# Kernel optimization log

Measured on AMD Instinct MI355X. Metric: run time of the kernel, lower is better.

The kernel has to match this reference:

```python
import jax, jax.numpy as jnp
import numpy as np

N = 50000     # nodes
E = 800000    # edges (before self-loops)
DIN = 128     # input feature dim
DH = 16       # per-head hidden dim (layer 1)
H = 8         # heads (layer 1)
DOUT = 64     # output classes (layer 2, heads=1)


def setup_inputs() -> dict:
    key = jax.random.key(0)
    ks = jax.random.split(key, 10)
    def rn(k, shape, scale=0.1):
        return jax.random.normal(k, shape, dtype=jnp.float32) * scale
    x = jax.random.normal(ks[0], (N, DIN), dtype=jnp.float32)
    edge_index = jax.random.randint(ks[1], (2, E), 0, N, dtype=jnp.int64)
    return {
        "x": x,
        "edge_index": edge_index,
        "W1": rn(ks[2], (DIN, H * DH)),
        "a_src1": rn(ks[3], (H, DH)),
        "a_dst1": rn(ks[4], (H, DH)),
        "b1": jnp.zeros((H * DH,), jnp.float32),
        "W2": rn(ks[5], (H * DH, DOUT)),
        "a_src2": rn(ks[6], (1, DOUT)),
        "a_dst2": rn(ks[7], (1, DOUT)),
        "b2": jnp.zeros((DOUT,), jnp.float32),
    }


def gat_conv(x, src, dst, W, a_src, a_dst, b, heads, out_dim):
    """PyG-style GATConv: edge attention + segment softmax over dst + scatter-add."""
    n = x.shape[0]
    h = (x @ W).reshape(n, heads, out_dim)                 # [N, H, D]
    alpha_src = jnp.sum(h * a_src, axis=-1)                # [N, H]
    alpha_dst = jnp.sum(h * a_dst, axis=-1)                # [N, H]
    e = jax.nn.leaky_relu(alpha_src[src] + alpha_dst[dst], 0.2)  # [Etot, H]
    # numerically-stable segment softmax grouped by destination node
    m = jax.ops.segment_max(e, dst, num_segments=n)        # [N, H]
    ex = jnp.exp(e - m[dst])
    s = jax.ops.segment_sum(ex, dst, num_segments=n)       # [N, H]
    alpha = ex / (s[dst] + 1e-16)                          # [Etot, H]
    msg = h[src] * alpha[..., None]                        # [Etot, H, D]
    out = jax.ops.segment_sum(msg, dst, num_segments=n)    # [N, H, D]
    return out.reshape(n, heads * out_dim) + b


def reference(x, W1, a_src1, a_dst1, b1, W2, a_src2, a_dst2, b2, edge_index):
    # eval mode: F.dropout(p=0.6, training=False) is identity
    loop = jnp.arange(N, dtype=edge_index.dtype)
    src = jnp.concatenate([edge_index[0], loop])  # add_self_loops=True (PyG default)
    dst = jnp.concatenate([edge_index[1], loop])
    h = gat_conv(x, src, dst, W1, a_src1, a_dst1, b1, H, DH)
    h = jax.nn.elu(h)
    h = gat_conv(h, src, dst, W2, a_src2, a_dst2, b2, 1, DOUT)
    return (h, jax.nn.log_softmax(h, axis=1))
```

## Files before the change

kernel.cpp:

```cpp
#include <hip/hip_runtime.h>

#define NN 50000
#define EE 800000
#define ET (EE + NN)
#define NCH ((NN + 255) / 256)
#define DEGB ((ET + 255) / 256)
#define WPB ((128 * 128 + 128 * 64 + 255) / 256)
#define GEMB ((NN + 63) / 64)

typedef unsigned short ushort_t;
using bf16x8 = __attribute__((ext_vector_type(8))) short;
using f32x4  = __attribute__((ext_vector_type(4))) float;

__device__ __forceinline__ float bf2f(ushort_t u) {
    return __uint_as_float(((unsigned int)u) << 16);
}
__device__ __forceinline__ ushort_t f2bf(float f) {
    unsigned int u = __float_as_uint(f);
    u += 0x7fffu + ((u >> 16) & 1u);
    return (ushort_t)(u >> 16);
}
__device__ __forceinline__ float lrelu(float e) {
    return fmaxf(e, 0.f) + 0.2f * fminf(e, 0.f);
}
__device__ __forceinline__ float ldf(const void* p, int i, bool f32) {
    return f32 ? ((const float*)p)[i] : bf2f(((const ushort_t*)p)[i]);
}

__device__ __forceinline__ bool sniff_f32(const unsigned int* __restrict__ xw) {
    int lane = threadIdx.x & 63;
    float v = __uint_as_float(xw[lane]);
    float a = fabsf(v);
    bool ok = (a > 1e-6f && a < 1e6f) || v == 0.f;
    unsigned long long m = __ballot(ok);
    return __popcll(m) >= 48;
}
__device__ __forceinline__ bool sniff_i64(const int* __restrict__ eiw) {
    int lane = threadIdx.x & 63;
    unsigned long long m = __ballot(eiw[2 * lane + 1] != 0);
    return __popcll(m) <= 4;
}

__device__ __forceinline__ void edge_sd(const int* ei, int i, bool i64, int& s, int& d) {
    if (i < EE) {
        if (i64) { s = ei[2 * i]; d = ei[2 * (EE + i)]; }
        else     { s = ei[i];     d = ei[EE + i]; }
    } else {
        s = d = i - EE;
    }
}
__device__ __forceinline__ int edge_d(const int* ei, int i, bool i64) {
    if (i < EE) return i64 ? ei[2 * (EE + i)] : ei[EE + i];
    return i - EE;
}

__global__ __launch_bounds__(256) void prep_kernel(const int* __restrict__ ei, int* __restrict__ deg8,
                                                   int* __restrict__ rank,
                                                   const unsigned int* __restrict__ xw,
                                                   const void* W1v, const void* W2v,
                                                   ushort_t* __restrict__ Wt1, ushort_t* __restrict__ Wt2) {
    int b = blockIdx.x;
    if (b < DEGB) {
        bool i64 = sniff_i64(ei);
        int i = b * 256 + threadIdx.x;
        if (i >= ET) return;
        int g = b & 7;
        int d = edge_d(ei, i, i64);
        rank[i] = atomicAdd(&deg8[(size_t)g * NN + d], 1);
    } else {
        bool f32 = sniff_f32(xw);
        int i = (b - DEGB) * 256 + threadIdx.x;
        if (i < 128 * 128) {
            int k = i >> 7, nc = i & 127;
            ushort_t v = f32 ? f2bf(((const float*)W1v)[i]) : ((const ushort_t*)W1v)[i];
            Wt1[nc * 128 + k] = v;
        }
        int j = i - 128 * 128;
        if (j >= 0 && j < 128 * 64) {
            int k = j >> 6, nc = j & 63;
            ushort_t v = f32 ? f2bf(((const float*)W2v)[j]) : ((const ushort_t*)W2v)[j];
            Wt2[nc * 128 + k] = v;
        }
    }
}

#define FLG_A (1ull << 62)

__global__ __launch_bounds__(256) void scan_kernel(int* __restrict__ deg8, int* __restrict__ rowptr,
                                                   unsigned long long* __restrict__ state) {
    __shared__ int wsum[4];
    __shared__ int bpref;
    int b = blockIdx.x;
    int t = threadIdx.x;
    int node = b * 256 + t;
    int lane = t & 63, wid = t >> 6;
    int dv[8];
    int v = 0;
    if (node < NN) {
        #pragma unroll
        for (int g = 0; g < 8; ++g) {
            dv[g] = deg8[(size_t)g * NN + node];
            v += dv[g];
        }
    }
    int x = v;
    #pragma unroll
    for (int off = 1; off < 64; off <<= 1) {
        int y = __shfl_up(x, off);
        if (lane >= off) x += y;
    }
    if (lane == 63) wsum[wid] = x;
    __syncthreads();
    if (t < 4) {
        int s = wsum[t];
        #pragma unroll
        for (int off = 1; off < 4; off <<= 1) {
            int y = __shfl_up(s, off);
            if (t >= off) s += y;
        }
        wsum[t] = s;
    }
    __syncthreads();
    int total = wsum[3];
    if (t == 0) atomicExch(&state[b], FLG_A | (unsigned long long)(unsigned)total);
    if (t < 64) {
        int p = 0;
        #pragma unroll
        for (int w = 0; w < (NCH + 63) / 64; ++w) {
            int j = w * 64 + t;
            unsigned long long sv = 0;
            if (j < b) {
                do { sv = atomicAdd(&state[j], 0ull); __builtin_amdgcn_s_sleep(1); } while (!(sv >> 62));
            }
            p += (int)(unsigned)(sv & 0xffffffffull);
        }
        #pragma unroll
        for (int off = 1; off < 64; off <<= 1) p += __shfl_xor(p, off);
        if (t == 0) bpref = p;
    }
    __syncthreads();
    int excl = x - v + ((wid > 0) ? wsum[wid - 1] : 0);
    if (node < NN) {
        int run = bpref + excl;
        rowptr[node] = run;
        #pragma unroll
        for (int g = 0; g < 8; ++g) {
            deg8[(size_t)g * NN + node] = run;
            run += dv[g];
        }
    }
    if (b == NCH - 1 && t == 0) rowptr[NN] = bpref + total;
}

template <bool AEXT, int NCOL, int NH>
__device__ __forceinline__ void mgemm_body(int bid, const void* Av, const ushort_t* __restrict__ Wt,
                                           const void* a_src, const void* a_dst,
                                           ushort_t* __restrict__ outb, float* __restrict__ asrc,
                                           float* __restrict__ adst, int n, bool f32) {
    constexpr int K = 128;
    constexpr int NCT = NCOL / 16;
    bool af32 = AEXT && f32;
    int t = threadIdx.x;
    int lane = t & 63, wid = t >> 6;
    int m = lane & 15, quad = lane >> 4;
    int rbase = bid * 64 + wid * 16;
    int row = rbase + m;
    bool rok = row < n;

    bf16x8 af[4];
    if (rok) {
        if (!af32) {
            const ushort_t* ap = (const ushort_t*)Av + (size_t)row * K + quad * 8;
            #pragma unroll
            for (int kk = 0; kk < 4; ++kk) af[kk] = *(const bf16x8*)(ap + kk * 32);
        } else {
            const float* ap = (const float*)Av + (size_t)row * K + quad * 8;
            #pragma unroll
            for (int kk = 0; kk < 4; ++kk) {
                float4 q0 = *(const float4*)(ap + kk * 32);
                float4 q1 = *(const float4*)(ap + kk * 32 + 4);
                bf16x8 v;
                v[0] = (short)f2bf(q0.x); v[1] = (short)f2bf(q0.y);
                v[2] = (short)f2bf(q0.z); v[3] = (short)f2bf(q0.w);
                v[4] = (short)f2bf(q1.x); v[5] = (short)f2bf(q1.y);
                v[6] = (short)f2bf(q1.z); v[7] = (short)f2bf(q1.w);
                af[kk] = v;
            }
        }
    } else {
        #pragma unroll
        for (int kk = 0; kk < 4; ++kk) af[kk] = (bf16x8){0, 0, 0, 0, 0, 0, 0, 0};
    }

    f32x4 acc[NCT];
    #pragma unroll
    for (int c = 0; c < NCT; ++c) acc[c] = (f32x4){0.f, 0.f, 0.f, 0.f};

    const ushort_t* wp = Wt + (size_t)m * K + quad * 8;
    #pragma unroll
    for (int c = 0; c < NCT; ++c) {
        const ushort_t* wc = wp + (size_t)c * 16 * K;
        #pragma unroll
        for (int kk = 0; kk < 4; ++kk) {
            bf16x8 bf = *(const bf16x8*)(wc + kk * 32);
            acc[c] = __builtin_amdgcn_mfma_f32_16x16x32_bf16(af[kk], bf, acc[c], 0, 0, 0);
        }
    }

    int orow0 = rbase + quad * 4;
    #pragma unroll
    for (int c = 0; c < NCT; ++c) {
        #pragma unroll
        for (int r = 0; r < 4; ++r) {
            int orow = orow0 + r;
            if (orow < n) outb[(size_t)orow * NCOL + c * 16 + m] = f2bf(acc[c][r]);
        }
    }

    if (NH == 8) {
        #pragma unroll
        for (int c = 0; c < NCT; ++c) {
            float as = ldf(a_src, c * 16 + m, f32);
            float ad = ldf(a_dst, c * 16 + m, f32);
            float ps[4], pd[4];
            #pragma unroll
            for (int r = 0; r < 4; ++r) { ps[r] = acc[c][r] * as; pd[r] = acc[c][r] * ad; }
            #pragma unroll
            for (int stp = 1; stp < 16; stp <<= 1) {
                #pragma unroll
                for (int r = 0; r < 4; ++r) {
                    ps[r] += __shfl_xor(ps[r], stp);
                    pd[r] += __shfl_xor(pd[r], stp);
                }
            }
            if (m == 0) {
                #pragma unroll
                for (int r = 0; r < 4; ++r) {
                    int orow = orow0 + r;
                    if (orow < n) {
                        asrc[(size_t)orow * 8 + c] = ps[r];
                        adst[(size_t)orow * 8 + c] = pd[r];
                    }
                }
            }
        }
    } else {
        float ps[4] = {0.f, 0.f, 0.f, 0.f}, pd[4] = {0.f, 0.f, 0.f, 0.f};
        #pragma unroll
        for (int c = 0; c < NCT; ++c) {
            float as = ldf(a_src, c * 16 + m, f32);
            float ad = ldf(a_dst, c * 16 + m, f32);
            #pragma unroll
            for (int r = 0; r < 4; ++r) {
                ps[r] = fmaf(acc[c][r], as, ps[r]);
                pd[r] = fmaf(acc[c][r], ad, pd[r]);
            }
        }
        #pragma unroll
        for (int stp = 1; stp < 16; stp <<= 1) {
            #pragma unroll
            for (int r = 0; r < 4; ++r) {
                ps[r] += __shfl_xor(ps[r], stp);
                pd[r] += __shfl_xor(pd[r], stp);
            }
        }
        if (m == 0) {
            #pragma unroll
            for (int r = 0; r < 4; ++r) {
                int orow = orow0 + r;
                if (orow < n) { asrc[orow] = ps[r]; adst[orow] = pd[r]; }
            }
        }
    }
}

__global__ __launch_bounds__(256) void gemm1_fill_kernel(const void* xv, const ushort_t* __restrict__ Wt1,
                                                         const void* as1, const void* ad1,
                                                         ushort_t* __restrict__ h1b,
                                                         float* __restrict__ asrc1, float* __restrict__ adst1,
                                                         const int* __restrict__ ei,
                                                         const int* __restrict__ deg8off,
                                                         const int* __restrict__ rank, int* __restrict__ col) {
    if (blockIdx.x < GEMB) {
        bool f32 = sniff_f32((const unsigned int*)xv);
        mgemm_body<true, 128, 8>(blockIdx.x, xv, Wt1, as1, ad1, h1b, asrc1, adst1, NN, f32);
        return;
    }
    int bb = blockIdx.x - GEMB;
    bool i64 = sniff_i64(ei);
    int i = bb * 256 + threadIdx.x;
    if (i >= ET) return;
    int g = bb & 7;
    int s, d;
    edge_sd(ei, i, i64, s, d);
    col[deg8off[(size_t)g * NN + d] + rank[i]] = s;
}

__global__ __launch_bounds__(256) void mgemm2_kernel(const void* Av, const ushort_t* __restrict__ Wt,
                                                     const void* a_src, const void* a_dst,
                                                     ushort_t* __restrict__ outb, float* __restrict__ asrc,
                                                     float* __restrict__ adst, const unsigned int* __restrict__ xw) {
    bool f32 = sniff_f32(xw);
    mgemm_body<false, 64, 1>(blockIdx.x, Av, Wt, a_src, a_dst, outb, asrc, adst, NN, f32);
}

__global__ __launch_bounds__(256) void agg1_kernel(const unsigned int* __restrict__ xw,
                                                   const int* __restrict__ rowptr, const int* __restrict__ col,
                                                   const ushort_t* __restrict__ h1b,
                                                   const float* __restrict__ asrc, const float* __restrict__ adst,
                                                   const void* b1, ushort_t* __restrict__ hmidb) {
    __shared__ float wle[4][8 * 72];
    __shared__ int loff[4][64];
    bool f32 = sniff_f32(xw);
    int lane = threadIdx.x & 63, wid = threadIdx.x >> 6;
    int d = blockIdx.x * 4 + wid;
    if (d >= NN) return;
    int start = rowptr[d], end = rowptr[d + 1];
    int sub = lane & 15;
    int eg  = lane >> 4;
    int hB  = sub >> 1;
    const float4* dp = (const float4*)(adst + (size_t)d * 8);
    float4 ad0 = dp[0], ad1 = dp[1];
    const char* hb = (const char*)h1b + sub * 16;
    float acc[8] = {0.f, 0.f, 0.f, 0.f, 0.f, 0.f, 0.f, 0.f};
    float ssum = 0.f;
    for (int chunk = start; chunk < end; chunk += 64) {
        int cnt = min(64, end - chunk);
        int c = (chunk + lane < end) ? col[chunk + lane] : 0;
        loff[wid][lane] = c << 8;
        if (lane < cnt) {
            const float4* ap = (const float4*)(asrc + (size_t)c * 8);
            float4 s0 = ap[0], s1 = ap[1];
            wle[wid][0 * 72 + lane] = __expf(lrelu(s0.x + ad0.x));
            wle[wid][1 * 72 + lane] = __expf(lrelu(s0.y + ad0.y));
            wle[wid][2 * 72 + lane] = __expf(lrelu(s0.z + ad0.z));
            wle[wid][3 * 72 + lane] = __expf(lrelu(s0.w + ad0.w));
            wle[wid][4 * 72 + lane] = __expf(lrelu(s1.x + ad1.x));
            wle[wid][5 * 72 + lane] = __expf(lrelu(s1.y + ad1.y));
            wle[wid][6 * 72 + lane] = __expf(lrelu(s1.z + ad1.z));
            wle[wid][7 * 72 + lane] = __expf(lrelu(s1.w + ad1.w));
        } else {
            #pragma unroll
            for (int h = 0; h < 8; ++h) wle[wid][h * 72 + lane] = 0.f;
        }
        int niter = (cnt + 3) >> 2;
        #pragma unroll 4
        for (int jj = 0; jj < niter; ++jj) {
            int j = jj * 4 + eg;
            int off = loff[wid][j];
            float ex = wle[wid][hB * 72 + j];
            uint4 hv = *(const uint4*)(hb + off);
            ssum += ex;
            acc[0] = fmaf(ex, __uint_as_float(hv.x << 16), acc[0]);
            acc[1] = fmaf(ex, __uint_as_float(hv.x & 0xffff0000u), acc[1]);
            acc[2] = fmaf(ex, __uint_as_float(hv.y << 16), acc[2]);
            acc[3] = fmaf(ex, __uint_as_float(hv.y & 0xffff0000u), acc[3]);
            acc[4] = fmaf(ex, __uint_as_float(hv.z << 16), acc[4]);
            acc[5] = fmaf(ex, __uint_as_float(hv.z & 0xffff0000u), acc[5]);
            acc[6] = fmaf(ex, __uint_as_float(hv.w << 16), acc[6]);
            acc[7] = fmaf(ex, __uint_as_float(hv.w & 0xffff0000u), acc[7]);
        }
    }
    #pragma unroll
    for (int off = 16; off < 64; off <<= 1) {
        ssum += __shfl_xor(ssum, off);
        #pragma unroll
        for (int k = 0; k < 8; ++k) acc[k] += __shfl_xor(acc[k], off);
    }
    if (eg == 0) {
        float inv = 1.f / (ssum + 1e-16f);
        uint4 pk;
        unsigned int pw[4];
        #pragma unroll
        for (int k = 0; k < 4; ++k) {
            float o0 = fmaf(acc[2 * k],     inv, ldf(b1, sub * 8 + 2 * k,     f32));
            float o1 = fmaf(acc[2 * k + 1], inv, ldf(b1, sub * 8 + 2 * k + 1, f32));
            o0 = (o0 > 0.f) ? o0 : (__expf(o0) - 1.f);
            o1 = (o1 > 0.f) ? o1 : (__expf(o1) - 1.f);
            pw[k] = ((unsigned int)f2bf(o1) << 16) | (unsigned int)f2bf(o0);
        }
        pk.x = pw[0]; pk.y = pw[1]; pk.z = pw[2]; pk.w = pw[3];
        *(uint4*)(hmidb + (size_t)d * 128 + sub * 8) = pk;
    }
}

__global__ __launch_bounds__(256) void agg2_kernel(const unsigned int* __restrict__ xw,
                                                   const int* __restrict__ rowptr, const int* __restrict__ col,
                                                   const ushort_t* __restrict__ h2b,
                                                   const float* __restrict__ asrc, const float* __restrict__ adst,
                                                   const void* b2, float* __restrict__ out) {
    __shared__ float wle[4][64];
    __shared__ int loff[4][64];
    bool f32 = sniff_f32(xw);
    int lane = threadIdx.x & 63, wid = threadIdx.x >> 6;
    int d = blockIdx.x * 4 + wid;
    if (d >= NN) return;
    int start = rowptr[d], end = rowptr[d + 1];
    int sub = lane & 7;
    int eg  = lane >> 3;
    float ad = adst[d];
    const char* hb = (const char*)h2b + sub * 16;
    float acc[8] = {0.f, 0.f, 0.f, 0.f, 0.f, 0.f, 0.f, 0.f};
    float ssum = 0.f;
    for (int chunk = start; chunk < end; chunk += 64) {
        int cnt = min(64, end - chunk);
        int c = (chunk + lane < end) ? col[chunk + lane] : 0;
        loff[wid][lane] = c << 7;
        float e = 0.f;
        if (lane < cnt) e = __expf(lrelu(asrc[c] + ad));
        wle[wid][lane] = e;
        int niter = (cnt + 7) >> 3;
        #pragma unroll 2
        for (int jj = 0; jj < niter; ++jj) {
            int j = jj * 8 + eg;
            int off = loff[wid][j];
            float ex = wle[wid][j];
            uint4 hv = *(const uint4*)(hb + off);
            ssum += ex;
            acc[0] = fmaf(ex, __uint_as_float(hv.x << 16), acc[0]);
            acc[1] = fmaf(ex, __uint_as_float(hv.x & 0xffff0000u), acc[1]);
            acc[2] = fmaf(ex, __uint_as_float(hv.y << 16), acc[2]);
            acc[3] = fmaf(ex, __uint_as_float(hv.y & 0xffff0000u), acc[3]);
            acc[4] = fmaf(ex, __uint_as_float(hv.z << 16), acc[4]);
            acc[5] = fmaf(ex, __uint_as_float(hv.z & 0xffff0000u), acc[5]);
            acc[6] = fmaf(ex, __uint_as_float(hv.w << 16), acc[6]);
            acc[7] = fmaf(ex, __uint_as_float(hv.w & 0xffff0000u), acc[7]);
        }
    }
    #pragma unroll
    for (int off = 8; off < 64; off <<= 1) {
        ssum += __shfl_xor(ssum, off);
        #pragma unroll
        for (int k = 0; k < 8; ++k) acc[k] += __shfl_xor(acc[k], off);
    }
    if (eg == 0) {
        float inv = 1.f / (ssum + 1e-16f);
        float o[8];
        #pragma unroll
        for (int k = 0; k < 8; ++k) o[k] = fmaf(acc[k], inv, ldf(b2, sub * 8 + k, f32));
        float mm = o[0];
        #pragma unroll
        for (int k = 1; k < 8; ++k) mm = fmaxf(mm, o[k]);
        #pragma unroll
        for (int off = 1; off < 8; off <<= 1) mm = fmaxf(mm, __shfl_xor(mm, off));
        float ts = 0.f;
        #pragma unroll
        for (int k = 0; k < 8; ++k) ts += __expf(o[k] - mm);
        #pragma unroll
        for (int off = 1; off < 8; off <<= 1) ts += __shfl_xor(ts, off);
        float lg = mm + __logf(ts);
        float4 w0, w1, l0, l1;
        w0.x = o[0]; w0.y = o[1]; w0.z = o[2]; w0.w = o[3];
        w1.x = o[4]; w1.y = o[5]; w1.z = o[6]; w1.w = o[7];
        l0.x = o[0] - lg; l0.y = o[1] - lg; l0.z = o[2] - lg; l0.w = o[3] - lg;
        l1.x = o[4] - lg; l1.y = o[5] - lg; l1.z = o[6] - lg; l1.w = o[7] - lg;
        float* op = out + (size_t)d * 64 + sub * 8;
        *(float4*)op = w0;
        *(float4*)(op + 4) = w1;
        float* lp = out + (size_t)NN * 64 + (size_t)d * 64 + sub * 8;
        *(float4*)lp = l0;
        *(float4*)(lp + 4) = l1;
    }
}

extern "C" void kernel_launch(void* const* d_in, const int* in_sizes, int n_in,
                              void* d_out, int out_size, void* d_ws, size_t ws_size,
                              hipStream_t stream) {
    const void* x   = d_in[0];
    const int*  ei  = (const int*)d_in[1];
    const void* W1  = d_in[2];
    const void* as1 = d_in[3];
    const void* ad1 = d_in[4];
    const void* b1  = d_in[5];
    const void* W2  = d_in[6];
    const void* as2 = d_in[7];
    const void* ad2 = d_in[8];
    const void* b2  = d_in[9];
    float* out = (float*)d_out;

    char* w = (char*)d_ws;
    auto alloc = [&](size_t bytes) {
        void* p = (void*)w;
        w += (bytes + 255) & ~(size_t)255;
        return p;
    };
    int* deg8     = (int*)alloc((size_t)8 * NN * 4 + 4096);
    unsigned long long* state = (unsigned long long*)((char*)deg8 + (size_t)8 * NN * 4);
    int* rowptr   = (int*)alloc((size_t)(NN + 1) * 4);
    int* rank     = (int*)alloc((size_t)ET * 4);
    int* colx     = (int*)alloc((size_t)ET * 4);
    ushort_t* Wt1 = (ushort_t*)alloc((size_t)128 * 128 * 2);
    ushort_t* Wt2 = (ushort_t*)alloc((size_t)64 * 128 * 2);
    ushort_t* h1b = (ushort_t*)alloc((size_t)NN * 128 * 2);
    float* asrc1  = (float*)alloc((size_t)NN * 8 * 4);
    float* adst1  = (float*)alloc((size_t)NN * 8 * 4);
    ushort_t* hmidb = (ushort_t*)alloc((size_t)NN * 128 * 2);
    ushort_t* h2b = (ushort_t*)alloc((size_t)NN * 64 * 2);
    float* asrc2  = (float*)alloc((size_t)NN * 4);
    float* adst2  = (float*)alloc((size_t)NN * 4);

    hipMemsetAsync(deg8, 0, (size_t)8 * NN * 4 + (size_t)NCH * 8, stream);

    prep_kernel<<<DEGB + WPB, 256, 0, stream>>>(ei, deg8, rank, (const unsigned int*)x, W1, W2, Wt1, Wt2);
    scan_kernel<<<NCH, 256, 0, stream>>>(deg8, rowptr, state);
    gemm1_fill_kernel<<<GEMB + DEGB, 256, 0, stream>>>(x, Wt1, as1, ad1, h1b, asrc1, adst1,
                                                       ei, deg8, rank, colx);
    agg1_kernel<<<(NN + 3) / 4, 256, 0, stream>>>((const unsigned int*)x, rowptr, colx, h1b,
                                                  asrc1, adst1, b1, hmidb);
    mgemm2_kernel<<<GEMB, 256, 0, stream>>>((const void*)hmidb, Wt2, as2, ad2, h2b, asrc2, adst2,
                                            (const unsigned int*)x);
    agg2_kernel<<<(NN + 3) / 4, 256, 0, stream>>>((const unsigned int*)x, rowptr, colx, h2b,
                                                  asrc2, adst2, b2, out);
}
```

Before: 252.0 us.

## Split layer-1 aggregation into per-edge alpha pass and head-planar gather

Layer-1 aggregation is split into two kernels. The first computes normalized attention coefficients per edge and head and stores them as bf16 planes. The second runs one block per (node group, head) and gathers from a head-planar copy of h1 that the GEMM now writes, so each head's gather footprint is 32 bytes per node. The aim is to improve cache locality for the random gather by working through one head's features at a time. In exchange it adds an extra launch, a 13.6 MB alpha buffer written and read back, eight reloads of col per node, and a redundant exp recomputation for long rows.

New measurement: 404.8 us. +60.6%, slower.

```diff
diff --git a/kernel.cpp b/kernel.cpp
--- a/kernel.cpp
+++ b/kernel.cpp
@@ -7,6 +7,7 @@
 #define DEGB ((ET + 255) / 256)
 #define WPB ((128 * 128 + 128 * 64 + 255) / 256)
 #define GEMB ((NN + 63) / 64)
+#define NODB ((NN + 3) / 4)
 
 typedef unsigned short ushort_t;
 using bf16x8 = __attribute__((ext_vector_type(8))) short;
@@ -152,7 +153,7 @@
     if (b == NCH - 1 && t == 0) rowptr[NN] = bpref + total;
 }
 
-template <bool AEXT, int NCOL, int NH>
+template <bool AEXT, int NCOL, int NH, bool PLANE>
 __device__ __forceinline__ void mgemm_body(int bid, const void* Av, const ushort_t* __restrict__ Wt,
                                            const void* a_src, const void* a_dst,
                                            ushort_t* __restrict__ outb, float* __restrict__ asrc,
@@ -213,7 +214,10 @@
         #pragma unroll
         for (int r = 0; r < 4; ++r) {
             int orow = orow0 + r;
-            if (orow < n) outb[(size_t)orow * NCOL + c * 16 + m] = f2bf(acc[c][r]);
+            if (orow < n) {
+                if (PLANE) outb[((size_t)c * n + orow) * 16 + m] = f2bf(acc[c][r]);
+                else       outb[(size_t)orow * NCOL + c * 16 + m] = f2bf(acc[c][r]);
+            }
         }
     }
 
@@ -276,14 +280,14 @@
 
 __global__ __launch_bounds__(256) void gemm1_fill_kernel(const void* xv, const ushort_t* __restrict__ Wt1,
                                                          const void* as1, const void* ad1,
-                                                         ushort_t* __restrict__ h1b,
+                                                         ushort_t* __restrict__ h1p,
                                                          float* __restrict__ asrc1, float* __restrict__ adst1,
                                                          const int* __restrict__ ei,
                                                          const int* __restrict__ deg8off,
                                                          const int* __restrict__ rank, int* __restrict__ col) {
     if (blockIdx.x < GEMB) {
         bool f32 = sniff_f32((const unsigned int*)xv);
-        mgemm_body<true, 128, 8>(blockIdx.x, xv, Wt1, as1, ad1, h1b, asrc1, adst1, NN, f32);
+        mgemm_body<true, 128, 8, true>(blockIdx.x, xv, Wt1, as1, ad1, h1p, asrc1, adst1, NN, f32);
         return;
     }
     int bb = blockIdx.x - GEMB;
@@ -301,86 +305,143 @@
                                                      ushort_t* __restrict__ outb, float* __restrict__ asrc,
                                                      float* __restrict__ adst, const unsigned int* __restrict__ xw) {
     bool f32 = sniff_f32(xw);
-    mgemm_body<false, 64, 1>(blockIdx.x, Av, Wt, a_src, a_dst, outb, asrc, adst, NN, f32);
-}
-
-__global__ __launch_bounds__(256) void agg1_kernel(const unsigned int* __restrict__ xw,
-                                                   const int* __restrict__ rowptr, const int* __restrict__ col,
-                                                   const ushort_t* __restrict__ h1b,
-                                                   const float* __restrict__ asrc, const float* __restrict__ adst,
-                                                   const void* b1, ushort_t* __restrict__ hmidb) {
-    __shared__ float wle[4][8 * 72];
-    __shared__ int loff[4][64];
-    bool f32 = sniff_f32(xw);
+    mgemm_body<false, 64, 1, false>(blockIdx.x, Av, Wt, a_src, a_dst, outb, asrc, adst, NN, f32);
+}
+
+__global__ __launch_bounds__(256) void alpha1_kernel(const int* __restrict__ rowptr, const int* __restrict__ col,
+                                                     const float* __restrict__ asrc, const float* __restrict__ adst,
+                                                     ushort_t* __restrict__ aplane) {
     int lane = threadIdx.x & 63, wid = threadIdx.x >> 6;
     int d = blockIdx.x * 4 + wid;
     if (d >= NN) return;
     int start = rowptr[d], end = rowptr[d + 1];
-    int sub = lane & 15;
-    int eg  = lane >> 4;
-    int hB  = sub >> 1;
     const float4* dp = (const float4*)(adst + (size_t)d * 8);
     float4 ad0 = dp[0], ad1 = dp[1];
-    const char* hb = (const char*)h1b + sub * 16;
-    float acc[8] = {0.f, 0.f, 0.f, 0.f, 0.f, 0.f, 0.f, 0.f};
-    float ssum = 0.f;
+    float ss[8] = {0.f, 0.f, 0.f, 0.f, 0.f, 0.f, 0.f, 0.f};
+    float ex0[8];
     for (int chunk = start; chunk < end; chunk += 64) {
-        int cnt = min(64, end - chunk);
-        int c = (chunk + lane < end) ? col[chunk + lane] : 0;
-        loff[wid][lane] = c << 8;
-        if (lane < cnt) {
+        int idx = chunk + lane;
+        float e[8];
+        if (idx < end) {
+            int c = col[idx];
             const float4* ap = (const float4*)(asrc + (size_t)c * 8);
             float4 s0 = ap[0], s1 = ap[1];
-            wle[wid][0 * 72 + lane] = __expf(lrelu(s0.x + ad0.x));
-            wle[wid][1 * 72 + lane] = __expf(lrelu(s0.y + ad0.y));
-            wle[wid][2 * 72 + lane] = __expf(lrelu(s0.z + ad0.z));
-            wle[wid][3 * 72 + lane] = __expf(lrelu(s0.w + ad0.w));
-            wle[wid][4 * 72 + lane] = __expf(lrelu(s1.x + ad1.x));
-            wle[wid][5 * 72 + lane] = __expf(lrelu(s1.y + ad1.y));
-            wle[wid][6 * 72 + lane] = __expf(lrelu(s1.z + ad1.z));
-            wle[wid][7 * 72 + lane] = __expf(lrelu(s1.w + ad1.w));
+            e[0] = __expf(lrelu(s0.x + ad0.x));
+            e[1] = __expf(lrelu(s0.y + ad0.y));
+            e[2] = __expf(lrelu(s0.z + ad0.z));
+            e[3] = __expf(lrelu(s0.w + ad0.w));
+            e[4] = __expf(lrelu(s1.x + ad1.x));
+            e[5] = __expf(lrelu(s1.y + ad1.y));
+            e[6] = __expf(lrelu(s1.z + ad1.z));
+            e[7] = __expf(lrelu(s1.w + ad1.w));
         } else {
             #pragma unroll
-            for (int h = 0; h < 8; ++h) wle[wid][h * 72 + lane] = 0.f;
-        }
-        int niter = (cnt + 3) >> 2;
+            for (int k = 0; k < 8; ++k) e[k] = 0.f;
+        }
+        #pragma unroll
+        for (int k = 0; k < 8; ++k) ss[k] += e[k];
+        if (chunk == start) {
+            #pragma unroll
+            for (int k = 0; k < 8; ++k) ex0[k] = e[k];
+        }
+    }
+    #pragma unroll
+    for (int off = 1; off < 64; off <<= 1) {
+        #pragma unroll
+        for (int k = 0; k < 8; ++k) ss[k] += __shfl_xor(ss[k], off);
+    }
+    float inv[8];
+    #pragma unroll
+    for (int k = 0; k < 8; ++k) inv[k] = 1.f / (ss[k] + 1e-16f);
+    {
+        int idx = start + lane;
+        if (idx < end) {
+            #pragma unroll
+            for (int k = 0; k < 8; ++k)
+                aplane[(size_t)k * ET + idx] = f2bf(ex0[k] * inv[k]);
+        }
+    }
+    for (int chunk = start + 64; chunk < end; chunk += 64) {
+        int idx = chunk + lane;
+        if (idx < end) {
+            int c = col[idx];
+            const float4* ap = (const float4*)(asrc + (size_t)c * 8);
+            float4 s0 = ap[0], s1 = ap[1];
+            float e[8];
+            e[0] = __expf(lrelu(s0.x + ad0.x));
+            e[1] = __expf(lrelu(s0.y + ad0.y));
+            e[2] = __expf(lrelu(s0.z + ad0.z));
+            e[3] = __expf(lrelu(s0.w + ad0.w));
+            e[4] = __expf(lrelu(s1.x + ad1.x));
+            e[5] = __expf(lrelu(s1.y + ad1.y));
+            e[6] = __expf(lrelu(s1.z + ad1.z));
+            e[7] = __expf(lrelu(s1.w + ad1.w));
+            #pragma unroll
+            for (int k = 0; k < 8; ++k)
+                aplane[(size_t)k * ET + idx] = f2bf(e[k] * inv[k]);
+        }
+    }
+}
+
+__global__ __launch_bounds__(256) void agg1b_kernel(const unsigned int* __restrict__ xw,
+                                                    const int* __restrict__ rowptr, const int* __restrict__ col,
+                                                    const ushort_t* __restrict__ h1p,
+                                                    const ushort_t* __restrict__ aplane,
+                                                    const void* b1, ushort_t* __restrict__ hmidb) {
+    __shared__ float wal[4][64];
+    __shared__ int loff[4][64];
+    bool f32 = sniff_f32(xw);
+    int lane = threadIdx.x & 63, wid = threadIdx.x >> 6;
+    int h = blockIdx.x & 7;
+    int d = (blockIdx.x >> 3) * 4 + wid;
+    if (d >= NN) return;
+    int start = rowptr[d], end = rowptr[d + 1];
+    int el = lane >> 2, dl = lane & 3;
+    const char* pb = (const char*)(h1p + (size_t)h * NN * 16) + dl * 8;
+    const ushort_t* ap = aplane + (size_t)h * ET;
+    float a0 = 0.f, a1 = 0.f, a2 = 0.f, a3 = 0.f;
+    for (int chunk = start; chunk < end; chunk += 64) {
+        int idx = chunk + lane;
+        int cnt = min(64, end - chunk);
+        int c = (idx < end) ? __builtin_nontemporal_load(&col[idx]) : 0;
+        loff[wid][lane] = c << 5;
+        float av = 0.f;
+        if (lane < cnt) av = bf2f(__builtin_nontemporal_load(&ap[idx]));
+        wal[wid][lane] = av;
+        int niter = (cnt + 15) >> 4;
         #pragma unroll 4
         for (int jj = 0; jj < niter; ++jj) {
-            int j = jj * 4 + eg;
+            int j = jj * 16 + el;
             int off = loff[wid][j];
-            float ex = wle[wid][hB * 72 + j];
-            uint4 hv = *(const uint4*)(hb + off);
-            ssum += ex;
-            acc[0] = fmaf(ex, __uint_as_float(hv.x << 16), acc[0]);
-            acc[1] = fmaf(ex, __uint_as_float(hv.x & 0xffff0000u), acc[1]);
-            acc[2] = fmaf(ex, __uint_as_float(hv.y << 16), acc[2]);
-            acc[3] = fmaf(ex, __uint_as_float(hv.y & 0xffff0000u), acc[3]);
-            acc[4] = fmaf(ex, __uint_as_float(hv.z << 16), acc[4]);
-            acc[5] = fmaf(ex, __uint_as_float(hv.z & 0xffff0000u), acc[5]);
-            acc[6] = fmaf(ex, __uint_as_float(hv.w << 16), acc[6]);
-            acc[7] = fmaf(ex, __uint_as_float(hv.w & 0xffff0000u), acc[7]);
-        }
-    }
-    #pragma unroll
-    for (int off = 16; off < 64; off <<= 1) {
-        ssum += __shfl_xor(ssum, off);
-        #pragma unroll
-        for (int k = 0; k < 8; ++k) acc[k] += __shfl_xor(acc[k], off);
-    }
-    if (eg == 0) {
-        float inv = 1.f / (ssum + 1e-16f);
-        uint4 pk;
-        unsigned int pw[4];
-        #pragma unroll
-        for (int k = 0; k < 4; ++k) {
-            float o0 = fmaf(acc[2 * k],     inv, ldf(b1, sub * 8 + 2 * k,     f32));
-            float o1 = fmaf(acc[2 * k + 1], inv, ldf(b1, sub * 8 + 2 * k + 1, f32));
-            o0 = (o0 > 0.f) ? o0 : (__expf(o0) - 1.f);
-            o1 = (o1 > 0.f) ? o1 : (__expf(o1) - 1.f);
-            pw[k] = ((unsigned int)f2bf(o1) << 16) | (unsigned int)f2bf(o0);
-        }
-        pk.x = pw[0]; pk.y = pw[1]; pk.z = pw[2]; pk.w = pw[3];
-        *(uint4*)(hmidb + (size_t)d * 128 + sub * 8) = pk;
+            float a = wal[wid][j];
+            uint2 hv = *(const uint2*)(pb + off);
+            a0 = fmaf(a, __uint_as_float(hv.x << 16), a0);
+            a1 = fmaf(a, __uint_as_float(hv.x & 0xffff0000u), a1);
+            a2 = fmaf(a, __uint_as_float(hv.y << 16), a2);
+            a3 = fmaf(a, __uint_as_float(hv.y & 0xffff0000u), a3);
+        }
+    }
+    #pragma unroll
+    for (int off = 4; off < 64; off <<= 1) {
+        a0 += __shfl_xor(a0, off);
+        a1 += __shfl_xor(a1, off);
+        a2 += __shfl_xor(a2, off);
+        a3 += __shfl_xor(a3, off);
+    }
+    if (el == 0) {
+        int db = h * 16 + dl * 4;
+        float o0 = a0 + ldf(b1, db + 0, f32);
+        float o1 = a1 + ldf(b1, db + 1, f32);
+        float o2 = a2 + ldf(b1, db + 2, f32);
+        float o3 = a3 + ldf(b1, db + 3, f32);
+        o0 = (o0 > 0.f) ? o0 : (__expf(o0) - 1.f);
+        o1 = (o1 > 0.f) ? o1 : (__expf(o1) - 1.f);
+        o2 = (o2 > 0.f) ? o2 : (__expf(o2) - 1.f);
+        o3 = (o3 > 0.f) ? o3 : (__expf(o3) - 1.f);
+        uint2 pk;
+        pk.x = ((unsigned int)f2bf(o1) << 16) | (unsigned int)f2bf(o0);
+        pk.y = ((unsigned int)f2bf(o3) << 16) | (unsigned int)f2bf(o2);
+        *(uint2*)(hmidb + (size_t)d * 128 + db) = pk;
     }
 }
 
@@ -491,9 +552,10 @@
     int* colx     = (int*)alloc((size_t)ET * 4);
     ushort_t* Wt1 = (ushort_t*)alloc((size_t)128 * 128 * 2);
     ushort_t* Wt2 = (ushort_t*)alloc((size_t)64 * 128 * 2);
-    ushort_t* h1b = (ushort_t*)alloc((size_t)NN * 128 * 2);
+    ushort_t* h1p = (ushort_t*)alloc((size_t)8 * NN * 16 * 2);
     float* asrc1  = (float*)alloc((size_t)NN * 8 * 4);
     float* adst1  = (float*)alloc((size_t)NN * 8 * 4);
+    ushort_t* aplane = (ushort_t*)alloc((size_t)8 * ET * 2);
     ushort_t* hmidb = (ushort_t*)alloc((size_t)NN * 128 * 2);
     ushort_t* h2b = (ushort_t*)alloc((size_t)NN * 64 * 2);
     float* asrc2  = (float*)alloc((size_t)NN * 4);
@@ -503,12 +565,13 @@
 
     prep_kernel<<<DEGB + WPB, 256, 0, stream>>>(ei, deg8, rank, (const unsigned int*)x, W1, W2, Wt1, Wt2);
     scan_kernel<<<NCH, 256, 0, stream>>>(deg8, rowptr, state);
-    gemm1_fill_kernel<<<GEMB + DEGB, 256, 0, stream>>>(x, Wt1, as1, ad1, h1b, asrc1, adst1,
+    gemm1_fill_kernel<<<GEMB + DEGB, 256, 0, stream>>>(x, Wt1, as1, ad1, h1p, asrc1, adst1,
                                                        ei, deg8, rank, colx);
-    agg1_kernel<<<(NN + 3) / 4, 256, 0, stream>>>((const unsigned int*)x, rowptr, colx, h1b,
-                                                  asrc1, adst1, b1, hmidb);
+    alpha1_kernel<<<NODB, 256, 0, stream>>>(rowptr, colx, asrc1, adst1, aplane);
+    agg1b_kernel<<<NODB * 8, 256, 0, stream>>>((const unsigned int*)x, rowptr, colx, h1p,
+                                               aplane, b1, hmidb);
     mgemm2_kernel<<<GEMB, 256, 0, stream>>>((const void*)hmidb, Wt2, as2, ad2, h2b, asrc2, adst2,
                                             (const unsigned int*)x);
-    agg2_kernel<<<(NN + 3) / 4, 256, 0, stream>>>((const unsigned int*)x, rowptr, colx, h2b,
-                                                  asrc2, adst2, b2, out);
-}
+    agg2_kernel<<<NODB, 256, 0, stream>>>((const unsigned int*)x, rowptr, colx, h2b,
+                                          asrc2, adst2, b2, out);
+}
```

## Fuse layer-2 GEMM into agg1 epilogue and vectorize edge preprocessing by 4

Applied to the files above, without the earlier changes.

The layer-2 projection and its attention logits are now computed inside agg1 with per-wave FMA dot products from shared memory. This removes the hmidb intermediate buffer, the mgemm2 launch and the round trip of the intermediate through memory. agg1's gather is restructured so each lane handles 2 features per edge, iterating serially over all edges instead of 4 edge groups with 8 features each. The degree-count and CSR-fill kernels now process 4 edges per thread with vector loads. The trade-offs are that the second GEMM runs on scalar FMAs instead of MFMA, and the agg1 inner loop has less edge-level parallelism.

Measured after the change: 373.9 us. +48.3%, slower.

```diff
diff --git a/kernel.cpp b/kernel.cpp
--- a/kernel.cpp
+++ b/kernel.cpp
@@ -4,9 +4,10 @@
 #define EE 800000
 #define ET (EE + NN)
 #define NCH ((NN + 255) / 256)
-#define DEGB ((ET + 255) / 256)
+#define DEG4B ((ET + 1023) / 1024)
 #define WPB ((128 * 128 + 128 * 64 + 255) / 256)
 #define GEMB ((NN + 63) / 64)
+#define NODB ((NN + 3) / 4)
 
 typedef unsigned short ushort_t;
 using bf16x8 = __attribute__((ext_vector_type(8))) short;
@@ -41,17 +42,35 @@
     return __popcll(m) <= 4;
 }
 
-__device__ __forceinline__ void edge_sd(const int* ei, int i, bool i64, int& s, int& d) {
-    if (i < EE) {
-        if (i64) { s = ei[2 * i]; d = ei[2 * (EE + i)]; }
-        else     { s = ei[i];     d = ei[EE + i]; }
+__device__ __forceinline__ void edge_d4(const int* __restrict__ ei, int i0, bool i64, int (&d)[4]) {
+    if (i0 < EE) {
+        if (i64) {
+            int4 r = *(const int4*)(ei + 2 * (size_t)(EE + i0));
+            int4 u = *(const int4*)(ei + 2 * (size_t)(EE + i0) + 4);
+            d[0] = r.x; d[1] = r.z; d[2] = u.x; d[3] = u.z;
+        } else {
+            int4 dv = *(const int4*)(ei + (size_t)EE + i0);
+            d[0] = dv.x; d[1] = dv.y; d[2] = dv.z; d[3] = dv.w;
+        }
     } else {
-        s = d = i - EE;
-    }
-}
-__device__ __forceinline__ int edge_d(const int* ei, int i, bool i64) {
-    if (i < EE) return i64 ? ei[2 * (EE + i)] : ei[EE + i];
-    return i - EE;
+        #pragma unroll
+        for (int e = 0; e < 4; ++e) d[e] = i0 + e - EE;
+    }
+}
+__device__ __forceinline__ void edge_s4(const int* __restrict__ ei, int i0, bool i64, int (&s)[4]) {
+    if (i0 < EE) {
+        if (i64) {
+            int4 p = *(const int4*)(ei + 2 * (size_t)i0);
+            int4 q = *(const int4*)(ei + 2 * (size_t)i0 + 4);
+            s[0] = p.x; s[1] = p.z; s[2] = q.x; s[3] = q.z;
+        } else {
+            int4 sv = *(const int4*)(ei + (size_t)i0);
+            s[0] = sv.x; s[1] = sv.y; s[2] = sv.z; s[3] = sv.w;
+        }
+    } else {
+        #pragma unroll
+        for (int e = 0; e < 4; ++e) s[e] = i0 + e - EE;
+    }
 }
 
 __global__ __launch_bounds__(256) void prep_kernel(const int* __restrict__ ei, int* __restrict__ deg8,
@@ -60,16 +79,26 @@
                                                    const void* W1v, const void* W2v,
                                                    ushort_t* __restrict__ Wt1, ushort_t* __restrict__ Wt2) {
     int b = blockIdx.x;
-    if (b < DEGB) {
+    if (b < DEG4B) {
         bool i64 = sniff_i64(ei);
-        int i = b * 256 + threadIdx.x;
-        if (i >= ET) return;
+        int i0 = (b * 256 + threadIdx.x) * 4;
+        if (i0 >= ET) return;
         int g = b & 7;
-        int d = edge_d(ei, i, i64);
-        rank[i] = atomicAdd(&deg8[(size_t)g * NN + d], 1);
+        int d[4], r[4];
+        edge_d4(ei, i0, i64, d);
+        #pragma unroll
+        for (int e = 0; e < 4; ++e)
+            if (i0 + e < ET) r[e] = atomicAdd(&deg8[(size_t)g * NN + d[e]], 1);
+        if (i0 + 3 < ET) {
+            int4 rv; rv.x = r[0]; rv.y = r[1]; rv.z = r[2]; rv.w = r[3];
+            *(int4*)(rank + i0) = rv;
+        } else {
+            #pragma unroll
+            for (int e = 0; e < 4; ++e) if (i0 + e < ET) rank[i0 + e] = r[e];
+        }
     } else {
         bool f32 = sniff_f32(xw);
-        int i = (b - DEGB) * 256 + threadIdx.x;
+        int i = (b - DEG4B) * 256 + threadIdx.x;
         if (i < 128 * 128) {
             int k = i >> 7, nc = i & 127;
             ushort_t v = f32 ? f2bf(((const float*)W1v)[i]) : ((const ushort_t*)W1v)[i];
@@ -152,24 +181,22 @@
     if (b == NCH - 1 && t == 0) rowptr[NN] = bpref + total;
 }
 
-template <bool AEXT, int NCOL, int NH>
-__device__ __forceinline__ void mgemm_body(int bid, const void* Av, const ushort_t* __restrict__ Wt,
-                                           const void* a_src, const void* a_dst,
-                                           ushort_t* __restrict__ outb, float* __restrict__ asrc,
-                                           float* __restrict__ adst, int n, bool f32) {
+__device__ __forceinline__ void mgemm1_body(int bid, const void* Av, const ushort_t* __restrict__ Wt,
+                                            const void* a_src, const void* a_dst,
+                                            ushort_t* __restrict__ outb, float* __restrict__ asrc,
+                                            float* __restrict__ adst, bool f32) {
     constexpr int K = 128;
-    constexpr int NCT = NCOL / 16;
-    bool af32 = AEXT && f32;
+    constexpr int NCT = 8;
     int t = threadIdx.x;
     int lane = t & 63, wid = t >> 6;
     int m = lane & 15, quad = lane >> 4;
     int rbase = bid * 64 + wid * 16;
     int row = rbase + m;
-    bool rok = row < n;
+    bool rok = row < NN;
 
     bf16x8 af[4];
     if (rok) {
-        if (!af32) {
+        if (!f32) {
             const ushort_t* ap = (const ushort_t*)Av + (size_t)row * K + quad * 8;
             #pragma unroll
             for (int kk = 0; kk < 4; ++kk) af[kk] = *(const bf16x8*)(ap + kk * 32);
@@ -213,49 +240,17 @@
         #pragma unroll
         for (int r = 0; r < 4; ++r) {
             int orow = orow0 + r;
-            if (orow < n) outb[(size_t)orow * NCOL + c * 16 + m] = f2bf(acc[c][r]);
-        }
-    }
-
-    if (NH == 8) {
-        #pragma unroll
-        for (int c = 0; c < NCT; ++c) {
-            float as = ldf(a_src, c * 16 + m, f32);
-            float ad = ldf(a_dst, c * 16 + m, f32);
-            float ps[4], pd[4];
-            #pragma unroll
-            for (int r = 0; r < 4; ++r) { ps[r] = acc[c][r] * as; pd[r] = acc[c][r] * ad; }
-            #pragma unroll
-            for (int stp = 1; stp < 16; stp <<= 1) {
-                #pragma unroll
-                for (int r = 0; r < 4; ++r) {
-                    ps[r] += __shfl_xor(ps[r], stp);
-                    pd[r] += __shfl_xor(pd[r], stp);
-                }
-            }
-            if (m == 0) {
-                #pragma unroll
-                for (int r = 0; r < 4; ++r) {
-                    int orow = orow0 + r;
-                    if (orow < n) {
-                        asrc[(size_t)orow * 8 + c] = ps[r];
-                        adst[(size_t)orow * 8 + c] = pd[r];
-                    }
-                }
-            }
-        }
-    } else {
-        float ps[4] = {0.f, 0.f, 0.f, 0.f}, pd[4] = {0.f, 0.f, 0.f, 0.f};
-        #pragma unroll
-        for (int c = 0; c < NCT; ++c) {
-            float as = ldf(a_src, c * 16 + m, f32);
-            float ad = ldf(a_dst, c * 16 + m, f32);
-            #pragma unroll
-            for (int r = 0; r < 4; ++r) {
-                ps[r] = fmaf(acc[c][r], as, ps[r]);
-                pd[r] = fmaf(acc[c][r], ad, pd[r]);
-            }
-        }
+            if (orow < NN) outb[(size_t)orow * 128 + c * 16 + m] = f2bf(acc[c][r]);
+        }
+    }
+
+    #pragma unroll
+    for (int c = 0; c < NCT; ++c) {
+        float as = ldf(a_src, c * 16 + m, f32);
+        float ad = ldf(a_dst, c * 16 + m, f32);
+        float ps[4], pd[4];
+        #pragma unroll
+        for (int r = 0; r < 4; ++r) { ps[r] = acc[c][r] * as; pd[r] = acc[c][r] * ad; }
         #pragma unroll
         for (int stp = 1; stp < 16; stp <<= 1) {
             #pragma unroll
@@ -268,7 +263,10 @@
             #pragma unroll
             for (int r = 0; r < 4; ++r) {
                 int orow = orow0 + r;
-                if (orow < n) { asrc[orow] = ps[r]; adst[orow] = pd[r]; }
+                if (orow < NN) {
+                    asrc[(size_t)orow * 8 + c] = ps[r];
+                    adst[(size_t)orow * 8 + c] = pd[r];
+                }
             }
         }
     }
@@ -283,47 +281,51 @@
                                                          const int* __restrict__ rank, int* __restrict__ col) {
     if (blockIdx.x < GEMB) {
         bool f32 = sniff_f32((const unsigned int*)xv);
-        mgemm_body<true, 128, 8>(blockIdx.x, xv, Wt1, as1, ad1, h1b, asrc1, adst1, NN, f32);
+        mgemm1_body(blockIdx.x, xv, Wt1, as1, ad1, h1b, asrc1, adst1, f32);
         return;
     }
     int bb = blockIdx.x - GEMB;
     bool i64 = sniff_i64(ei);
-    int i = bb * 256 + threadIdx.x;
-    if (i >= ET) return;
+    int i0 = (bb * 256 + threadIdx.x) * 4;
+    if (i0 >= ET) return;
     int g = bb & 7;
-    int s, d;
-    edge_sd(ei, i, i64, s, d);
-    col[deg8off[(size_t)g * NN + d] + rank[i]] = s;
-}
-
-__global__ __launch_bounds__(256) void mgemm2_kernel(const void* Av, const ushort_t* __restrict__ Wt,
-                                                     const void* a_src, const void* a_dst,
-                                                     ushort_t* __restrict__ outb, float* __restrict__ asrc,
-                                                     float* __restrict__ adst, const unsigned int* __restrict__ xw) {
-    bool f32 = sniff_f32(xw);
-    mgemm_body<false, 64, 1>(blockIdx.x, Av, Wt, a_src, a_dst, outb, asrc, adst, NN, f32);
+    int s[4], d[4];
+    edge_s4(ei, i0, i64, s);
+    edge_d4(ei, i0, i64, d);
+    if (i0 + 3 < ET) {
+        int4 rv = *(const int4*)(rank + i0);
+        int r[4] = {rv.x, rv.y, rv.z, rv.w};
+        #pragma unroll
+        for (int e = 0; e < 4; ++e)
+            col[deg8off[(size_t)g * NN + d[e]] + r[e]] = s[e];
+    } else {
+        #pragma unroll
+        for (int e = 0; e < 4; ++e)
+            if (i0 + e < ET) col[deg8off[(size_t)g * NN + d[e]] + rank[i0 + e]] = s[e];
+    }
 }
 
 __global__ __launch_bounds__(256) void agg1_kernel(const unsigned int* __restrict__ xw,
                                                    const int* __restrict__ rowptr, const int* __restrict__ col,
                                                    const ushort_t* __restrict__ h1b,
                                                    const float* __restrict__ asrc, const float* __restrict__ adst,
-                                                   const void* b1, ushort_t* __restrict__ hmidb) {
+                                                   const void* b1, const ushort_t* __restrict__ Wt2,
+                                                   const void* as2, const void* ad2,
+                                                   ushort_t* __restrict__ h2b,
+                                                   float* __restrict__ asrc2, float* __restrict__ adst2) {
     __shared__ float wle[4][8 * 72];
     __shared__ int loff[4][64];
+    __shared__ float hsm[4][128];
     bool f32 = sniff_f32(xw);
     int lane = threadIdx.x & 63, wid = threadIdx.x >> 6;
     int d = blockIdx.x * 4 + wid;
     if (d >= NN) return;
     int start = rowptr[d], end = rowptr[d + 1];
-    int sub = lane & 15;
-    int eg  = lane >> 4;
-    int hB  = sub >> 1;
+    int hB = lane >> 3;
     const float4* dp = (const float4*)(adst + (size_t)d * 8);
     float4 ad0 = dp[0], ad1 = dp[1];
-    const char* hb = (const char*)h1b + sub * 16;
-    float acc[8] = {0.f, 0.f, 0.f, 0.f, 0.f, 0.f, 0.f, 0.f};
-    float ssum = 0.f;
+    const char* hb = (const char*)h1b + lane * 4;
+    float acc0 = 0.f, acc1 = 0.f, ssum = 0.f;
     for (int chunk = start; chunk < end; chunk += 64) {
         int cnt = min(64, end - chunk);
         int c = (chunk + lane < end) ? col[chunk + lane] : 0;
@@ -339,49 +341,49 @@
             wle[wid][5 * 72 + lane] = __expf(lrelu(s1.y + ad1.y));
             wle[wid][6 * 72 + lane] = __expf(lrelu(s1.z + ad1.z));
             wle[wid][7 * 72 + lane] = __expf(lrelu(s1.w + ad1.w));
-        } else {
-            #pragma unroll
-            for (int h = 0; h < 8; ++h) wle[wid][h * 72 + lane] = 0.f;
-        }
-        int niter = (cnt + 3) >> 2;
-        #pragma unroll 4
-        for (int jj = 0; jj < niter; ++jj) {
-            int j = jj * 4 + eg;
+        }
+        #pragma unroll 8
+        for (int j = 0; j < cnt; ++j) {
             int off = loff[wid][j];
             float ex = wle[wid][hB * 72 + j];
-            uint4 hv = *(const uint4*)(hb + off);
+            unsigned int hv = *(const unsigned int*)(hb + off);
             ssum += ex;
-            acc[0] = fmaf(ex, __uint_as_float(hv.x << 16), acc[0]);
-            acc[1] = fmaf(ex, __uint_as_float(hv.x & 0xffff0000u), acc[1]);
-            acc[2] = fmaf(ex, __uint_as_float(hv.y << 16), acc[2]);
-            acc[3] = fmaf(ex, __uint_as_float(hv.y & 0xffff0000u), acc[3]);
-            acc[4] = fmaf(ex, __uint_as_float(hv.z << 16), acc[4]);
-            acc[5] = fmaf(ex, __uint_as_float(hv.z & 0xffff0000u), acc[5]);
-            acc[6] = fmaf(ex, __uint_as_float(hv.w << 16), acc[6]);
-            acc[7] = fmaf(ex, __uint_as_float(hv.w & 0xffff0000u), acc[7]);
-        }
-    }
-    #pragma unroll
-    for (int off = 16; off < 64; off <<= 1) {
-        ssum += __shfl_xor(ssum, off);
-        #pragma unroll
-        for (int k = 0; k < 8; ++k) acc[k] += __shfl_xor(acc[k], off);
-    }
-    if (eg == 0) {
-        float inv = 1.f / (ssum + 1e-16f);
-        uint4 pk;
-        unsigned int pw[4];
-        #pragma unroll
-        for (int k = 0; k < 4; ++k) {
-            float o0 = fmaf(acc[2 * k],     inv, ldf(b1, sub * 8 + 2 * k,     f32));
-            float o1 = fmaf(acc[2 * k + 1], inv, ldf(b1, sub * 8 + 2 * k + 1, f32));
-            o0 = (o0 > 0.f) ? o0 : (__expf(o0) - 1.f);
-            o1 = (o1 > 0.f) ? o1 : (__expf(o1) - 1.f);
-            pw[k] = ((unsigned int)f2bf(o1) << 16) | (unsigned int)f2bf(o0);
-        }
-        pk.x = pw[0]; pk.y = pw[1]; pk.z = pw[2]; pk.w = pw[3];
-        *(uint4*)(hmidb + (size_t)d * 128 + sub * 8) = pk;
-    }
+            acc0 = fmaf(ex, __uint_as_float(hv << 16), acc0);
+            acc1 = fmaf(ex, __uint_as_float(hv & 0xffff0000u), acc1);
+        }
+    }
+    float inv = 1.f / (ssum + 1e-16f);
+    float o0 = fmaf(acc0, inv, ldf(b1, lane * 2, f32));
+    float o1 = fmaf(acc1, inv, ldf(b1, lane * 2 + 1, f32));
+    o0 = (o0 > 0.f) ? o0 : (__expf(o0) - 1.f);
+    o1 = (o1 > 0.f) ? o1 : (__expf(o1) - 1.f);
+    hsm[wid][lane * 2] = o0;
+    hsm[wid][lane * 2 + 1] = o1;
+    const ushort_t* w2 = Wt2 + (size_t)lane * 128;
+    float h2 = 0.f;
+    #pragma unroll
+    for (int kk = 0; kk < 16; ++kk) {
+        bf16x8 wv = *(const bf16x8*)(w2 + kk * 8);
+        const float* hp = &hsm[wid][kk * 8];
+        h2 = fmaf(hp[0], bf2f((ushort_t)wv[0]), h2);
+        h2 = fmaf(hp[1], bf2f((ushort_t)wv[1]), h2);
+        h2 = fmaf(hp[2], bf2f((ushort_t)wv[2]), h2);
+        h2 = fmaf(hp[3], bf2f((ushort_t)wv[3]), h2);
+        h2 = fmaf(hp[4], bf2f((ushort_t)wv[4]), h2);
+        h2 = fmaf(hp[5], bf2f((ushort_t)wv[5]), h2);
+        h2 = fmaf(hp[6], bf2f((ushort_t)wv[6]), h2);
+        h2 = fmaf(hp[7], bf2f((ushort_t)wv[7]), h2);
+    }
+    float as = ldf(as2, lane, f32);
+    float ad = ldf(ad2, lane, f32);
+    float ps = h2 * as, pd = h2 * ad;
+    #pragma unroll
+    for (int off = 1; off < 64; off <<= 1) {
+        ps += __shfl_xor(ps, off);
+        pd += __shfl_xor(pd, off);
+    }
+    h2b[(size_t)d * 64 + lane] = f2bf(h2);
+    if (lane == 0) { asrc2[d] = ps; adst2[d] = pd; }
 }
 
 __global__ __launch_bounds__(256) void agg2_kernel(const unsigned int* __restrict__ xw,
@@ -494,21 +496,18 @@
     ushort_t* h1b = (ushort_t*)alloc((size_t)NN * 128 * 2);
     float* asrc1  = (float*)alloc((size_t)NN * 8 * 4);
     float* adst1  = (float*)alloc((size_t)NN * 8 * 4);
-    ushort_t* hmidb = (ushort_t*)alloc((size_t)NN * 128 * 2);
     ushort_t* h2b = (ushort_t*)alloc((size_t)NN * 64 * 2);
     float* asrc2  = (float*)alloc((size_t)NN * 4);
     float* adst2  = (float*)alloc((size_t)NN * 4);
 
     hipMemsetAsync(deg8, 0, (size_t)8 * NN * 4 + (size_t)NCH * 8, stream);
 
-    prep_kernel<<<DEGB + WPB, 256, 0, stream>>>(ei, deg8, rank, (const unsigned int*)x, W1, W2, Wt1, Wt2);
+    prep_kernel<<<DEG4B + WPB, 256, 0, stream>>>(ei, deg8, rank, (const unsigned int*)x, W1, W2, Wt1, Wt2);
     scan_kernel<<<NCH, 256, 0, stream>>>(deg8, rowptr, state);
-    gemm1_fill_kernel<<<GEMB + DEGB, 256, 0, stream>>>(x, Wt1, as1, ad1, h1b, asrc1, adst1,
-                                                       ei, deg8, rank, colx);
-    agg1_kernel<<<(NN + 3) / 4, 256, 0, stream>>>((const unsigned int*)x, rowptr, colx, h1b,
-                                                  asrc1, adst1, b1, hmidb);
-    mgemm2_kernel<<<GEMB, 256, 0, stream>>>((const void*)hmidb, Wt2, as2, ad2, h2b, asrc2, adst2,
-                                            (const unsigned int*)x);
-    agg2_kernel<<<(NN + 3) / 4, 256, 0, stream>>>((const unsigned int*)x, rowptr, colx, h2b,
-                                                  asrc2, adst2, b2, out);
-}
+    gemm1_fill_kernel<<<GEMB + DEG4B, 256, 0, stream>>>(x, Wt1, as1, ad1, h1b, asrc1, adst1,
+                                                        ei, deg8, rank, colx);
+    agg1_kernel<<<NODB, 256, 0, stream>>>((const unsigned int*)x, rowptr, colx, h1b,
+                                          asrc1, adst1, b1, Wt2, as2, ad2, h2b, asrc2, adst2);
+    agg2_kernel<<<NODB, 256, 0, stream>>>((const unsigned int*)x, rowptr, colx, h2b,
+                                          asrc2, adst2, b2, out);
+}
```
